# Kernel optimization log

Measured on AMD Instinct MI355X. Metric: run time of the kernel, lower is better.

The kernel has to match this reference:

```python
import jax, jax.numpy as jnp
import numpy as np

B, L, HID = 1, 2048, 4096
H, KV, D = 32, 2, 128
ROT = int(D * 0.5)  # partial rotary dims per head
THETA = 10000.0
SCALE = D ** -0.5


def _rope_tables(L, rot, theta):
    inv_freq = 1.0 / (theta ** (np.arange(0, rot, 2, dtype=np.float32) / rot))  # [rot/2]
    t = np.arange(L, dtype=np.float32)
    freqs = np.outer(t, inv_freq)  # [L, rot/2]
    return jnp.asarray(np.cos(freqs)), jnp.asarray(np.sin(freqs))


def setup_inputs() -> dict:
    key = jax.random.key(0)
    ks = jax.random.split(key, 8)
    s = HID ** -0.5
    x = jax.random.normal(ks[0], (B, L, HID), dtype=jnp.float32)
    Wq = jax.random.normal(ks[1], (HID, H * D), dtype=jnp.float32) * s
    Wk = jax.random.normal(ks[2], (HID, KV * D), dtype=jnp.float32) * s
    Wv = jax.random.normal(ks[3], (HID, KV * D), dtype=jnp.float32) * s
    Wo = jax.random.normal(ks[4], (H * D, HID), dtype=jnp.float32) * s
    bq = jax.random.normal(ks[5], (H * D,), dtype=jnp.float32) * 0.01
    bk = jax.random.normal(ks[6], (KV * D,), dtype=jnp.float32) * 0.01
    bv = jax.random.normal(ks[7], (KV * D,), dtype=jnp.float32) * 0.01
    cos, sin = _rope_tables(L, ROT, THETA)
    # additive causal mask
    causal = jnp.tril(jnp.ones((L, L), dtype=bool))
    attention_mask = jnp.where(causal, 0.0, -1e9)[None, None].astype(jnp.float32)
    return {"x": x, "Wq": Wq, "bq": bq, "Wk": Wk, "bk": bk, "Wv": Wv, "bv": bv,
            "Wo": Wo, "cos": cos, "sin": sin, "attention_mask": attention_mask}


def _apply_rope(t, cos, sin):
    # t: [B, h, L, D]; rotary on first ROT dims, pass-through on the rest
    t_rot, t_pass = t[..., :ROT], t[..., ROT:]
    x1, x2 = t_rot[..., : ROT // 2], t_rot[..., ROT // 2:]
    c = cos[None, None]  # [1,1,L,ROT/2]
    s = sin[None, None]
    rot = jnp.concatenate([x1 * c - x2 * s, x2 * c + x1 * s], axis=-1)
    return jnp.concatenate([rot, t_pass], axis=-1)


def reference(x, Wq, bq, Wk, bk, Wv, bv, Wo, cos, sin, attention_mask):
    Bx, Lx, _ = x.shape
    q = (x @ Wq + bq).reshape(Bx, Lx, H, D).transpose(0, 2, 1, 3)   # [B,H,L,D]
    k = (x @ Wk + bk).reshape(Bx, Lx, KV, D).transpose(0, 2, 1, 3)  # [B,KV,L,D]
    v = (x @ Wv + bv).reshape(Bx, Lx, KV, D).transpose(0, 2, 1, 3)
    q = _apply_rope(q, cos, sin)
    k = _apply_rope(k, cos, sin)
    # GQA: repeat KV heads
    rep = H // KV
    k = jnp.repeat(k, rep, axis=1)  # [B,H,L,D]
    v = jnp.repeat(v, rep, axis=1)
    w = jnp.einsum('bhqd,bhkd->bhqk', q, k) * SCALE + attention_mask
    w = jax.nn.softmax(w, axis=-1)
    o = jnp.einsum('bhqk,bhkd->bhqd', w, v)
    o = o.transpose(0, 2, 1, 3).reshape(Bx, Lx, H * D)
    return o @ Wo
```

## Files before the change

kernel.cpp:

```cpp
#include <hip/hip_runtime.h>
#include <stdint.h>

#define L_SEQ 2048
#define HID   4096
#define NH    32
#define NKV   2
#define DH    128
#define NQKV  4608
#define QSCALE 0.088388347648318447f

typedef __bf16 bf16x8 __attribute__((ext_vector_type(8)));
typedef float  f32x4  __attribute__((ext_vector_type(4)));

__device__ __forceinline__ unsigned short f2bf(float f) {
  union { float f; unsigned u; } cv; cv.f = f;
  unsigned u = cv.u;
  return (unsigned short)((u + 0x7fffu + ((u >> 16) & 1u)) >> 16);
}
__device__ __forceinline__ float bf2f(unsigned short h) {
  union { unsigned u; float f; } cv; cv.u = (unsigned)h << 16; return cv.f;
}

#define GLL16(gsrc, ldst)                                                              \
  __builtin_amdgcn_global_load_lds(                                                    \
      (const __attribute__((address_space(1))) unsigned int*)(gsrc),                   \
      (__attribute__((address_space(3))) unsigned int*)(ldst), 16, 0, 0)

__global__ __launch_bounds__(256) void cast_bf16_kernel(const float* __restrict__ in,
                                                        unsigned short* __restrict__ out,
                                                        int n4) {
  int i = blockIdx.x * 256 + threadIdx.x;
  if (i >= n4) return;
  float4 v = reinterpret_cast<const float4*>(in)[i];
  ushort4 o;
  o.x = f2bf(v.x); o.y = f2bf(v.y); o.z = f2bf(v.z); o.w = f2bf(v.w);
  reinterpret_cast<ushort4*>(out)[i] = o;
}

__global__ __launch_bounds__(256) void transpose_cast_kernel(const float* __restrict__ in,
                                                             unsigned short* __restrict__ out,
                                                             int R, int C) {
  __shared__ float tile[32][33];
  int c0 = blockIdx.x * 32, r0 = blockIdx.y * 32;
  int tx = threadIdx.x, ty = threadIdx.y;
  #pragma unroll
  for (int i = ty; i < 32; i += 8)
    tile[i][tx] = in[(size_t)(r0 + i) * C + (c0 + tx)];
  __syncthreads();
  #pragma unroll
  for (int i = ty; i < 32; i += 8)
    out[(size_t)(c0 + i) * R + (r0 + tx)] = f2bf(tile[tx][i]);
}

#define TBM 128
#define TBN 128
#define TBK 64

template <int OUT_BF16>
__global__ __launch_bounds__(256, 2) void gemm128_kernel(const unsigned short* __restrict__ A,
                                                         const unsigned short* __restrict__ Bt,
                                                         void* __restrict__ Cv,
                                                         int M, int N, int K) {
  __shared__ __attribute__((aligned(16))) unsigned short As[2][TBM * TBK];
  __shared__ __attribute__((aligned(16))) unsigned short Bs[2][TBN * TBK];
  const int tid = threadIdx.x;
  const int wave = tid >> 6, lane = tid & 63;
  const int lg = lane >> 4, ll = lane & 15;
  const int wm = wave >> 1, wn = wave & 1;

  int gx = gridDim.x, nwg = gx * gridDim.y;
  int flat = blockIdx.y * gx + blockIdx.x;
  int bx = blockIdx.x, by = blockIdx.y;
  if ((nwg & 7) == 0) {
    int t = (flat & 7) * (nwg >> 3) + (flat >> 3);
    bx = t % gx; by = t / gx;
  }
  const int m0 = by * TBM, n0 = bx * TBN;

  f32x4 acc[4][4] = {};
  const int NT = K >> 6;

  auto stage = [&](int t, int buf) {
    const int k0 = t * TBK;
    #pragma unroll
    for (int i = 0; i < 4; ++i) {
      int ci  = (i * 4 + wave) * 64 + lane;
      int row = ci >> 3;
      int cg  = (ci & 7) ^ (row & 7);
      GLL16(A + (size_t)(m0 + row) * K + k0 + cg * 8, &As[buf][(i * 4 + wave) * 512]);
    }
    #pragma unroll
    for (int i = 0; i < 4; ++i) {
      int ci  = (i * 4 + wave) * 64 + lane;
      int row = ci >> 3;
      int cg  = (ci & 7) ^ (row & 7);
      GLL16(Bt + (size_t)(n0 + row) * K + k0 + cg * 8, &Bs[buf][(i * 4 + wave) * 512]);
    }
  };

  stage(0, 0);
  stage(1, 1);

  for (int t = 0; t < NT; ++t) {
    const int cur = t & 1;
    if (t + 1 < NT) asm volatile("s_waitcnt vmcnt(8)" ::: "memory");
    else            asm volatile("s_waitcnt vmcnt(0)" ::: "memory");
    __builtin_amdgcn_s_barrier();

    const unsigned short* Ac = &As[cur][0];
    const unsigned short* Bc = &Bs[cur][0];
    bf16x8 afr[2][4], bfr[2][4];
    #pragma unroll
    for (int kk = 0; kk < 2; ++kk)
      #pragma unroll
      for (int i = 0; i < 4; ++i) {
        int ra = wm * 64 + i * 16 + ll;
        afr[kk][i] = *reinterpret_cast<const bf16x8*>(
            &Ac[ra * 64 + (((kk * 4 + lg) ^ (ra & 7)) * 8)]);
        int rb = wn * 64 + i * 16 + ll;
        bfr[kk][i] = *reinterpret_cast<const bf16x8*>(
            &Bc[rb * 64 + (((kk * 4 + lg) ^ (rb & 7)) * 8)]);
      }
    asm volatile("s_waitcnt lgkmcnt(0)" ::: "memory");
    __builtin_amdgcn_s_barrier();
    if (t + 2 < NT) stage(t + 2, cur);

    __builtin_amdgcn_s_setprio(1);
    #pragma unroll
    for (int kk = 0; kk < 2; ++kk)
      #pragma unroll
      for (int i = 0; i < 4; ++i)
        #pragma unroll
        for (int j = 0; j < 4; ++j)
          acc[i][j] = __builtin_amdgcn_mfma_f32_16x16x32_bf16(afr[kk][i], bfr[kk][j],
                                                              acc[i][j], 0, 0, 0);
    __builtin_amdgcn_s_setprio(0);
  }

  #pragma unroll
  for (int i = 0; i < 4; ++i)
    #pragma unroll
    for (int j = 0; j < 4; ++j) {
      int col  = n0 + wn * 64 + j * 16 + ll;
      int rowb = m0 + wm * 64 + i * 16 + lg * 4;
      #pragma unroll
      for (int r = 0; r < 4; ++r) {
        size_t idx = (size_t)(rowb + r) * N + col;
        if (OUT_BF16) ((unsigned short*)Cv)[idx] = f2bf(acc[i][j][r]);
        else          ((float*)Cv)[idx]          = acc[i][j][r];
      }
    }
}

__global__ __launch_bounds__(128) void qkv_post_kernel(const unsigned short* __restrict__ qkv,
                                                       const float* __restrict__ bq,
                                                       const float* __restrict__ bk,
                                                       const float* __restrict__ bv,
                                                       const float* __restrict__ cosT,
                                                       const float* __restrict__ sinT,
                                                       unsigned short* __restrict__ qb,
                                                       unsigned short* __restrict__ kb,
                                                       unsigned short* __restrict__ vt) {
  int l = blockIdx.x, y = blockIdx.y, d = threadIdx.x;
  if (y < 34) {
    const bool isq = (y < 32);
    const int hh = isq ? y : (y - 32);
    const float* bias = isq ? bq : bk;
    size_t base = (size_t)l * NQKV + (isq ? 0 : 4096) + hh * DH;
    float v = bf2f(qkv[base + d]) + bias[hh * DH + d];
    float o;
    if (d < 32) {
      float x2 = bf2f(qkv[base + d + 32]) + bias[hh * DH + d + 32];
      o = v * cosT[l * 32 + d] - x2 * sinT[l * 32 + d];
    } else if (d < 64) {
      int i = d - 32;
      float x1 = bf2f(qkv[base + i]) + bias[hh * DH + i];
      o = v * cosT[l * 32 + i] + x1 * sinT[l * 32 + i];
    } else {
      o = v;
    }
    if (isq) qb[((size_t)hh * L_SEQ + l) * DH + d] = f2bf(o * QSCALE);
    else     kb[((size_t)hh * L_SEQ + l) * DH + d] = f2bf(o);
  } else {
    int g = y - 34;
    float o = bf2f(qkv[(size_t)l * NQKV + 4352 + g * DH + d]) + bv[g * DH + d];
    vt[((size_t)g * DH + d) * L_SEQ + l] = f2bf(o);
  }
}

__device__ __forceinline__ int p_addr(int row, int chunk) {
  return row * 72 + (((chunk + row + (row >> 2)) & 7) * 8);
}

__global__ __launch_bounds__(256) void attn_kernel(const unsigned short* __restrict__ qg,
                                                   const unsigned short* __restrict__ kb,
                                                   const unsigned short* __restrict__ vt,
                                                   unsigned short* __restrict__ ob) {
  __shared__ __attribute__((aligned(16))) unsigned short Ks[2][64 * 128];
  __shared__ __attribute__((aligned(16))) unsigned short Vs[2][128 * 64];
  __shared__ __attribute__((aligned(16))) unsigned short Ps[4][16 * 72];

  const int pair = blockIdx.x, h = blockIdx.y;
  const int g = h >> 4;
  const int tid = threadIdx.x, wave = tid >> 6, lane = tid & 63;
  const int lg = lane >> 4, ll = lane & 15;

  const int krow = (lane >> 4);
  const int kcg0 = (lane & 15);
  const int vrow = (lane >> 3);
  const int vcg0 = (lane & 7);

  #pragma unroll
  for (int seg = 0; seg < 2; ++seg) {
    const int qt = seg ? (31 - pair) : pair;
    const int q0 = qt * 64 + wave * 16;

    bf16x8 qf[4];
    #pragma unroll
    for (int f = 0; f < 4; ++f)
      qf[f] = *reinterpret_cast<const bf16x8*>(
          qg + ((size_t)h * L_SEQ + q0 + ll) * DH + f * 32 + lg * 8);

    f32x4 of[8] = {};
    float m[4]  = {-1e30f, -1e30f, -1e30f, -1e30f};
    float lsum[4] = {0.f, 0.f, 0.f, 0.f};

    const int kvN = qt + 1;
    int cur = 0;

    #pragma unroll
    for (int c = 0; c < 4; ++c) {
      int issue = wave * 4 + c;
      int rk = issue * 4 + krow;
      GLL16(kb + ((size_t)g * L_SEQ + rk) * DH + (kcg0 ^ (rk & 7)) * 8, &Ks[0][issue * 512]);
      int rv = issue * 8 + vrow;
      GLL16(vt + ((size_t)g * DH + rv) * L_SEQ + (vcg0 ^ (rv & 7)) * 8, &Vs[0][issue * 512]);
    }
    __syncthreads();

    for (int t = 0; t < kvN; ++t) {
      if (t + 1 < kvN) {
        int kv1 = (t + 1) * 64;
        #pragma unroll
        for (int c = 0; c < 4; ++c) {
          int issue = wave * 4 + c;
          int rk = issue * 4 + krow;
          GLL16(kb + ((size_t)g * L_SEQ + kv1 + rk) * DH + (kcg0 ^ (rk & 7)) * 8,
                &Ks[cur ^ 1][issue * 512]);
          int rv = issue * 8 + vrow;
          GLL16(vt + ((size_t)g * DH + rv) * L_SEQ + kv1 + (vcg0 ^ (rv & 7)) * 8,
                &Vs[cur ^ 1][issue * 512]);
        }
      }

      f32x4 s[4] = {};
      const unsigned short* Kc = &Ks[cur][0];
      #pragma unroll
      for (int cf = 0; cf < 4; ++cf) {
        bf16x8 kf[4];
        #pragma unroll
        for (int f = 0; f < 4; ++f) {
          int rk = cf * 16 + ll;
          int cc = (f * 4 + lg) ^ (rk & 7);
          kf[f] = *reinterpret_cast<const bf16x8*>(&Kc[rk * 128 + cc * 8]);
        }
        __builtin_amdgcn_s_setprio(1);
        #pragma unroll
        for (int f = 0; f < 4; ++f)
          s[cf] = __builtin_amdgcn_mfma_f32_16x16x32_bf16(qf[f], kf[f], s[cf], 0, 0, 0);
        __builtin_amdgcn_s_setprio(0);
      }

      if (t == qt) {
        #pragma unroll
        for (int cf = 0; cf < 4; ++cf)
          #pragma unroll
          for (int r = 0; r < 4; ++r)
            if (cf * 16 + ll > wave * 16 + lg * 4 + r) s[cf][r] = -1e30f;
      }

      float pmax[4];
      #pragma unroll
      for (int r = 0; r < 4; ++r)
        pmax[r] = fmaxf(fmaxf(s[0][r], s[1][r]), fmaxf(s[2][r], s[3][r]));
      bool ok = true;
      #pragma unroll
      for (int r = 0; r < 4; ++r) ok = ok && (pmax[r] - m[r] <= 8.f);
      if (!__all(ok)) {
        float alpha[4];
        #pragma unroll
        for (int r = 0; r < 4; ++r) {
          float mx = pmax[r];
          #pragma unroll
          for (int msk = 1; msk < 16; msk <<= 1) mx = fmaxf(mx, __shfl_xor(mx, msk));
          float mnew = fmaxf(m[r], mx);
          alpha[r] = __expf(m[r] - mnew);
          m[r] = mnew;
          lsum[r] *= alpha[r];
        }
        #pragma unroll
        for (int ds = 0; ds < 8; ++ds)
          #pragma unroll
          for (int r = 0; r < 4; ++r)
            of[ds][r] *= alpha[r];
      }
      #pragma unroll
      for (int cf = 0; cf < 4; ++cf)
        #pragma unroll
        for (int r = 0; r < 4; ++r) {
          s[cf][r] = __expf(s[cf][r] - m[r]);
          lsum[r] += s[cf][r];
        }

      unsigned short* pw = &Ps[wave][0];
      #pragma unroll
      for (int cf = 0; cf < 4; ++cf)
        #pragma unroll
        for (int r = 0; r < 4; ++r) {
          int rr = lg * 4 + r;
          int c  = cf * 16 + ll;
          pw[p_addr(rr, c >> 3) + (c & 7)] = f2bf(s[cf][r]);
        }
      bf16x8 pa[2];
      #pragma unroll
      for (int ks = 0; ks < 2; ++ks)
        pa[ks] = *reinterpret_cast<const bf16x8*>(&pw[p_addr(ll, ks * 4 + lg)]);

      const unsigned short* Vc = &Vs[cur][0];
      #pragma unroll
      for (int ds = 0; ds < 8; ++ds) {
        bf16x8 vf[2];
        #pragma unroll
        for (int ks = 0; ks < 2; ++ks) {
          int dl = ds * 16 + ll;
          int cc = (ks * 4 + lg) ^ (dl & 7);
          vf[ks] = *reinterpret_cast<const bf16x8*>(&Vc[dl * 64 + cc * 8]);
        }
        __builtin_amdgcn_s_setprio(1);
        #pragma unroll
        for (int ks = 0; ks < 2; ++ks)
          of[ds] = __builtin_amdgcn_mfma_f32_16x16x32_bf16(pa[ks], vf[ks], of[ds], 0, 0, 0);
        __builtin_amdgcn_s_setprio(0);
      }

      __syncthreads();
      cur ^= 1;
    }

    float inv[4];
    #pragma unroll
    for (int r = 0; r < 4; ++r) {
      float sum = lsum[r];
      #pragma unroll
      for (int msk = 1; msk < 16; msk <<= 1) sum += __shfl_xor(sum, msk);
      inv[r] = 1.f / sum;
    }
    #pragma unroll
    for (int ds = 0; ds < 8; ++ds)
      #pragma unroll
      for (int r = 0; r < 4; ++r) {
        int row = q0 + lg * 4 + r;
        ob[(size_t)row * (NH * DH) + h * DH + ds * 16 + ll] = f2bf(of[ds][r] * inv[r]);
      }
    __syncthreads();
  }
}

extern "C" void kernel_launch(void* const* d_in, const int* in_sizes, int n_in,
                              void* d_out, int out_size, void* d_ws, size_t ws_size,
                              hipStream_t stream) {
  (void)in_sizes; (void)n_in; (void)out_size; (void)ws_size;
  const float* x    = (const float*)d_in[0];
  const float* Wq   = (const float*)d_in[1];
  const float* bq   = (const float*)d_in[2];
  const float* Wk   = (const float*)d_in[3];
  const float* bk   = (const float*)d_in[4];
  const float* Wv   = (const float*)d_in[5];
  const float* bv   = (const float*)d_in[6];
  const float* Wo   = (const float*)d_in[7];
  const float* cosT = (const float*)d_in[8];
  const float* sinT = (const float*)d_in[9];

  char* ws = (char*)d_ws;
  size_t off = 0;
  auto alloc = [&](size_t bytes) { void* p = ws + off; off += (bytes + 255) & ~(size_t)255; return p; };
  unsigned short* xb     = (unsigned short*)alloc((size_t)L_SEQ * HID * 2);
  unsigned short* Wqkvt  = (unsigned short*)alloc((size_t)NQKV * HID * 2);
  unsigned short* Wot    = (unsigned short*)alloc((size_t)HID * HID * 2);
  unsigned short* qkvlin = (unsigned short*)alloc((size_t)L_SEQ * NQKV * 2);
  unsigned short* qbuf   = (unsigned short*)alloc((size_t)NH * L_SEQ * DH * 2);
  unsigned short* kbuf   = (unsigned short*)alloc((size_t)NKV * L_SEQ * DH * 2);
  unsigned short* vtb    = (unsigned short*)alloc((size_t)NKV * DH * L_SEQ * 2);
  unsigned short* attno  = (unsigned short*)alloc((size_t)L_SEQ * HID * 2);

  cast_bf16_kernel<<<(L_SEQ * HID / 4 + 255) / 256, 256, 0, stream>>>(x, xb, L_SEQ * HID / 4);
  transpose_cast_kernel<<<dim3(HID / 32, HID / 32), dim3(32, 8), 0, stream>>>(Wq, Wqkvt, HID, HID);
  transpose_cast_kernel<<<dim3(256 / 32, HID / 32), dim3(32, 8), 0, stream>>>(Wk, Wqkvt + (size_t)4096 * HID, HID, 256);
  transpose_cast_kernel<<<dim3(256 / 32, HID / 32), dim3(32, 8), 0, stream>>>(Wv, Wqkvt + (size_t)4352 * HID, HID, 256);
  transpose_cast_kernel<<<dim3(HID / 32, HID / 32), dim3(32, 8), 0, stream>>>(Wo, Wot, HID, HID);

  gemm128_kernel<1><<<dim3(NQKV / TBN, L_SEQ / TBM), 256, 0, stream>>>(xb, Wqkvt, qkvlin, L_SEQ, NQKV, HID);

  qkv_post_kernel<<<dim3(L_SEQ, 36), 128, 0, stream>>>(qkvlin, bq, bk, bv, cosT, sinT,
                                                       qbuf, kbuf, vtb);

  attn_kernel<<<dim3(16, NH), 256, 0, stream>>>(qbuf, kbuf, vtb, attno);

  gemm128_kernel<0><<<dim3(HID / TBN, L_SEQ / TBM), 256, 0, stream>>>(attno, Wot, (float*)d_out, L_SEQ, HID, HID);
}
```

Measured before the change: 363.8 us.

## Vectorize weight transpose, move GEMM barrier after MFMA, transpose S in attention

The weight transpose-cast kernel moves to 64x64 tiles with float4 loads and packed 32-bit bf16 stores, so it issues fewer, wider memory accesses. In the GEMM, the early lgkmcnt wait and barrier are removed, and the barrier plus next-stage prefetch now come after the MFMA block, so LDS fragment reads overlap with compute. In attention, S is computed as K·Q^T so each lane holds one query row. This makes the row max and sum cheaper (two cross-lane shuffles instead of four) and allows packed 8-byte P stores into a smaller swizzled LDS buffer. The risk is a data race: the compute phase no longer waits for LDS reads before the barrier, and the new P layout has to stay correct.

```diff
diff --git a/kernel.cpp b/kernel.cpp
--- a/kernel.cpp
+++ b/kernel.cpp
@@ -40,16 +40,26 @@
 __global__ __launch_bounds__(256) void transpose_cast_kernel(const float* __restrict__ in,
                                                              unsigned short* __restrict__ out,
                                                              int R, int C) {
-  __shared__ float tile[32][33];
-  int c0 = blockIdx.x * 32, r0 = blockIdx.y * 32;
-  int tx = threadIdx.x, ty = threadIdx.y;
+  __shared__ float tile[64][65];
+  const int c0 = blockIdx.x * 64, r0 = blockIdx.y * 64;
+  const int tid = threadIdx.x;
   #pragma unroll
-  for (int i = ty; i < 32; i += 8)
-    tile[i][tx] = in[(size_t)(r0 + i) * C + (c0 + tx)];
+  for (int it = 0; it < 4; ++it) {
+    int row = it * 16 + (tid >> 4);
+    float4 v = *reinterpret_cast<const float4*>(&in[(size_t)(r0 + row) * C + c0 + (tid & 15) * 4]);
+    tile[row][(tid & 15) * 4 + 0] = v.x;
+    tile[row][(tid & 15) * 4 + 1] = v.y;
+    tile[row][(tid & 15) * 4 + 2] = v.z;
+    tile[row][(tid & 15) * 4 + 3] = v.w;
+  }
   __syncthreads();
   #pragma unroll
-  for (int i = ty; i < 32; i += 8)
-    out[(size_t)(c0 + i) * R + (r0 + tx)] = f2bf(tile[tx][i]);
+  for (int it = 0; it < 8; ++it) {
+    int c  = it * 8 + (tid >> 5);
+    int rp = tid & 31;
+    unsigned u = (unsigned)f2bf(tile[2 * rp][c]) | ((unsigned)f2bf(tile[2 * rp + 1][c]) << 16);
+    *reinterpret_cast<unsigned*>(&out[(size_t)(c0 + c) * R + r0 + 2 * rp]) = u;
+  }
 }
 
 #define TBM 128
@@ -121,10 +131,6 @@
         bfr[kk][i] = *reinterpret_cast<const bf16x8*>(
             &Bc[rb * 64 + (((kk * 4 + lg) ^ (rb & 7)) * 8)]);
       }
-    asm volatile("s_waitcnt lgkmcnt(0)" ::: "memory");
-    __builtin_amdgcn_s_barrier();
-    if (t + 2 < NT) stage(t + 2, cur);
-
     __builtin_amdgcn_s_setprio(1);
     #pragma unroll
     for (int kk = 0; kk < 2; ++kk)
@@ -135,6 +141,9 @@
           acc[i][j] = __builtin_amdgcn_mfma_f32_16x16x32_bf16(afr[kk][i], bfr[kk][j],
                                                               acc[i][j], 0, 0, 0);
     __builtin_amdgcn_s_setprio(0);
+
+    __builtin_amdgcn_s_barrier();
+    if (t + 2 < NT) stage(t + 2, cur);
   }
 
   #pragma unroll
@@ -188,17 +197,13 @@
   }
 }
 
-__device__ __forceinline__ int p_addr(int row, int chunk) {
-  return row * 72 + (((chunk + row + (row >> 2)) & 7) * 8);
-}
-
 __global__ __launch_bounds__(256) void attn_kernel(const unsigned short* __restrict__ qg,
                                                    const unsigned short* __restrict__ kb,
                                                    const unsigned short* __restrict__ vt,
                                                    unsigned short* __restrict__ ob) {
   __shared__ __attribute__((aligned(16))) unsigned short Ks[2][64 * 128];
   __shared__ __attribute__((aligned(16))) unsigned short Vs[2][128 * 64];
-  __shared__ __attribute__((aligned(16))) unsigned short Ps[4][16 * 72];
+  __shared__ __attribute__((aligned(16))) unsigned short Ps[4][16 * 64];
 
   const int pair = blockIdx.x, h = blockIdx.y;
   const int g = h >> 4;
@@ -222,8 +227,7 @@
           qg + ((size_t)h * L_SEQ + q0 + ll) * DH + f * 32 + lg * 8);
 
     f32x4 of[8] = {};
-    float m[4]  = {-1e30f, -1e30f, -1e30f, -1e30f};
-    float lsum[4] = {0.f, 0.f, 0.f, 0.f};
+    float m = -1e30f, lsum = 0.f;
 
     const int kvN = qt + 1;
     int cur = 0;
@@ -267,7 +271,7 @@
         __builtin_amdgcn_s_setprio(1);
         #pragma unroll
         for (int f = 0; f < 4; ++f)
-          s[cf] = __builtin_amdgcn_mfma_f32_16x16x32_bf16(qf[f], kf[f], s[cf], 0, 0, 0);
+          s[cf] = __builtin_amdgcn_mfma_f32_16x16x32_bf16(kf[f], qf[f], s[cf], 0, 0, 0);
         __builtin_amdgcn_s_setprio(0);
       }
 
@@ -276,55 +280,50 @@
         for (int cf = 0; cf < 4; ++cf)
           #pragma unroll
           for (int r = 0; r < 4; ++r)
-            if (cf * 16 + ll > wave * 16 + lg * 4 + r) s[cf][r] = -1e30f;
-      }
-
-      float pmax[4];
-      #pragma unroll
-      for (int r = 0; r < 4; ++r)
-        pmax[r] = fmaxf(fmaxf(s[0][r], s[1][r]), fmaxf(s[2][r], s[3][r]));
-      bool ok = true;
-      #pragma unroll
-      for (int r = 0; r < 4; ++r) ok = ok && (pmax[r] - m[r] <= 8.f);
-      if (!__all(ok)) {
-        float alpha[4];
-        #pragma unroll
-        for (int r = 0; r < 4; ++r) {
-          float mx = pmax[r];
-          #pragma unroll
-          for (int msk = 1; msk < 16; msk <<= 1) mx = fmaxf(mx, __shfl_xor(mx, msk));
-          float mnew = fmaxf(m[r], mx);
-          alpha[r] = __expf(m[r] - mnew);
-          m[r] = mnew;
-          lsum[r] *= alpha[r];
-        }
+            if (cf * 16 + lg * 4 + r > wave * 16 + ll) s[cf][r] = -1e30f;
+      }
+
+      float pmax = -1e30f;
+      #pragma unroll
+      for (int cf = 0; cf < 4; ++cf)
+        #pragma unroll
+        for (int r = 0; r < 4; ++r) pmax = fmaxf(pmax, s[cf][r]);
+      if (!__all(pmax - m <= 8.f)) {
+        float mx = fmaxf(pmax, __shfl_xor(pmax, 16));
+        mx = fmaxf(mx, __shfl_xor(mx, 32));
+        float mnew = fmaxf(m, mx);
+        float alpha = __expf(m - mnew);
+        m = mnew;
+        lsum *= alpha;
+        float af[4];
+        #pragma unroll
+        for (int r = 0; r < 4; ++r) af[r] = __shfl(alpha, lg * 4 + r);
         #pragma unroll
         for (int ds = 0; ds < 8; ++ds)
           #pragma unroll
-          for (int r = 0; r < 4; ++r)
-            of[ds][r] *= alpha[r];
-      }
-      #pragma unroll
-      for (int cf = 0; cf < 4; ++cf)
-        #pragma unroll
-        for (int r = 0; r < 4; ++r) {
-          s[cf][r] = __expf(s[cf][r] - m[r]);
-          lsum[r] += s[cf][r];
-        }
+          for (int r = 0; r < 4; ++r) of[ds][r] *= af[r];
+      }
 
       unsigned short* pw = &Ps[wave][0];
-      #pragma unroll
-      for (int cf = 0; cf < 4; ++cf)
-        #pragma unroll
-        for (int r = 0; r < 4; ++r) {
-          int rr = lg * 4 + r;
-          int c  = cf * 16 + ll;
-          pw[p_addr(rr, c >> 3) + (c & 7)] = f2bf(s[cf][r]);
-        }
+      float psum = 0.f;
+      #pragma unroll
+      for (int cf = 0; cf < 4; ++cf) {
+        float p0 = __expf(s[cf][0] - m), p1 = __expf(s[cf][1] - m);
+        float p2 = __expf(s[cf][2] - m), p3 = __expf(s[cf][3] - m);
+        psum += (p0 + p1) + (p2 + p3);
+        uint2 w;
+        w.x = (unsigned)f2bf(p0) | ((unsigned)f2bf(p1) << 16);
+        w.y = (unsigned)f2bf(p2) | ((unsigned)f2bf(p3) << 16);
+        int chunk = (cf * 2 + (lg >> 1)) ^ (ll & 7);
+        *reinterpret_cast<uint2*>(&pw[ll * 64 + chunk * 8 + (lg & 1) * 4]) = w;
+      }
+      lsum += psum;
+
       bf16x8 pa[2];
       #pragma unroll
       for (int ks = 0; ks < 2; ++ks)
-        pa[ks] = *reinterpret_cast<const bf16x8*>(&pw[p_addr(ll, ks * 4 + lg)]);
+        pa[ks] = *reinterpret_cast<const bf16x8*>(
+            &pw[ll * 64 + (((ks * 4 + lg) ^ (ll & 7)) * 8)]);
 
       const unsigned short* Vc = &Vs[cur][0];
       #pragma unroll
@@ -347,20 +346,18 @@
       cur ^= 1;
     }
 
-    float inv[4];
-    #pragma unroll
-    for (int r = 0; r < 4; ++r) {
-      float sum = lsum[r];
-      #pragma unroll
-      for (int msk = 1; msk < 16; msk <<= 1) sum += __shfl_xor(sum, msk);
-      inv[r] = 1.f / sum;
-    }
+    float tot = lsum + __shfl_xor(lsum, 16);
+    tot += __shfl_xor(tot, 32);
+    float inv = 1.f / tot;
+    float invr[4];
+    #pragma unroll
+    for (int r = 0; r < 4; ++r) invr[r] = __shfl(inv, lg * 4 + r);
     #pragma unroll
     for (int ds = 0; ds < 8; ++ds)
       #pragma unroll
       for (int r = 0; r < 4; ++r) {
         int row = q0 + lg * 4 + r;
-        ob[(size_t)row * (NH * DH) + h * DH + ds * 16 + ll] = f2bf(of[ds][r] * inv[r]);
+        ob[(size_t)row * (NH * DH) + h * DH + ds * 16 + ll] = f2bf(of[ds][r] * invr[r]);
       }
     __syncthreads();
   }
@@ -394,10 +391,10 @@
   unsigned short* attno  = (unsigned short*)alloc((size_t)L_SEQ * HID * 2);
 
   cast_bf16_kernel<<<(L_SEQ * HID / 4 + 255) / 256, 256, 0, stream>>>(x, xb, L_SEQ * HID / 4);
-  transpose_cast_kernel<<<dim3(HID / 32, HID / 32), dim3(32, 8), 0, stream>>>(Wq, Wqkvt, HID, HID);
-  transpose_cast_kernel<<<dim3(256 / 32, HID / 32), dim3(32, 8), 0, stream>>>(Wk, Wqkvt + (size_t)4096 * HID, HID, 256);
-  transpose_cast_kernel<<<dim3(256 / 32, HID / 32), dim3(32, 8), 0, stream>>>(Wv, Wqkvt + (size_t)4352 * HID, HID, 256);
-  transpose_cast_kernel<<<dim3(HID / 32, HID / 32), dim3(32, 8), 0, stream>>>(Wo, Wot, HID, HID);
+  transpose_cast_kernel<<<dim3(HID / 64, HID / 64), 256, 0, stream>>>(Wq, Wqkvt, HID, HID);
+  transpose_cast_kernel<<<dim3(256 / 64, HID / 64), 256, 0, stream>>>(Wk, Wqkvt + (size_t)4096 * HID, HID, 256);
+  transpose_cast_kernel<<<dim3(256 / 64, HID / 64), 256, 0, stream>>>(Wv, Wqkvt + (size_t)4352 * HID, HID, 256);
+  transpose_cast_kernel<<<dim3(HID / 64, HID / 64), 256, 0, stream>>>(Wo, Wot, HID, HID);
 
   gemm128_kernel<1><<<dim3(NQKV / TBN, L_SEQ / TBM), 256, 0, stream>>>(xb, Wqkvt, qkvlin, L_SEQ, NQKV, HID);
 
```

After: 352.7 us. 3.0% less time.
